# Kernel tuning notes

Measured on AMD Instinct MI355X. Metric: run time of the kernel, lower is better.

## Reference

```python
import jax, jax.numpy as jnp
import numpy as np

LAMB = 0.1
SIZE_AVERAGE = True


def setup_inputs() -> dict:
    key = jax.random.key(0)
    k1, k2 = jax.random.split(key)
    N, D = 8192, 4096
    inp = jax.random.normal(k1, (N, D), dtype=jnp.float32)
    target = jax.random.normal(k2, (N, D), dtype=jnp.float32)
    return {"input": inp, "target": target}


def _drae_loss(inp, target, lamb=LAMB, size_average=SIZE_AVERAGE):
    # Per-sample squared reconstruction error: Err[n] = sum_d (inp - target)^2
    err = (inp - target).reshape(inp.shape[0], -1)
    Err = jnp.sum(err * err, axis=1)                      # [N]
    N = Err.shape[0]
    sErr = jnp.sort(Err)                                  # ascending

    # Prefix sums replace the original O(N^2) Python scan.
    cs = jnp.cumsum(sErr)                                 # [N]
    cs2 = jnp.cumsum(sErr * sErr)                         # [N]
    total, total2 = cs[-1], cs2[-1]
    nf = jnp.asarray(N, sErr.dtype)
    allMean = total / nf
    Sb = total2 - nf * allMean * allMean                  # sum (e - allMean)^2

    # Candidate splits: inlier count k = 1..N-1 (loop index i = k-1).
    k = jnp.arange(1, N, dtype=sErr.dtype)                # [N-1]
    csk, cs2k = cs[:-1], cs2[:-1]
    Sw1 = cs2k - csk * csk / k                            # within-inlier scatter
    Sw2 = (total2 - cs2k) - (total - csk) ** 2 / (nf - k) # within-outlier scatter
    obj = (Sw1 + Sw2) / Sb                                # Fisher-style ratio

    i = jnp.argmin(obj)                                   # first min, like strict '<'
    optObj = obj[i]
    T = (i + 1).astype(sErr.dtype)                        # inlier count
    inlier_sum = cs[i]

    out = inlier_sum / T if size_average else inlier_sum
    return out + lamb * optObj


def reference(input, target):
    return _drae_loss(input, target)
```

## Files before the change

### kernel.cpp

```cpp
#include <hip/hip_runtime.h>

#define NROWS 8192
#define NCOLS 4096
#define LAMB  0.1

typedef unsigned int u32;
typedef unsigned long long u64;

__global__ __launch_bounds__(256) void rowerr_kernel(const float* __restrict__ inp,
                                                     const float* __restrict__ tgt,
                                                     float* __restrict__ err) {
    const int row = blockIdx.x;
    const float4* a = reinterpret_cast<const float4*>(inp + (size_t)row * NCOLS);
    const float4* b = reinterpret_cast<const float4*>(tgt + (size_t)row * NCOLS);
    const int t = threadIdx.x;

    float acc = 0.f;
#pragma unroll
    for (int c = 0; c < 4; ++c) {
        float4 va = a[t + c * 256];
        float4 vb = b[t + c * 256];
        float dx = va.x - vb.x;
        float dy = va.y - vb.y;
        float dz = va.z - vb.z;
        float dw = va.w - vb.w;
        acc += dx * dx + dy * dy + dz * dz + dw * dw;
    }

#pragma unroll
    for (int off = 32; off > 0; off >>= 1) acc += __shfl_down(acc, off, 64);

    __shared__ float ws[4];
    const int lane = t & 63, wv = t >> 6;
    if (lane == 0) ws[wv] = acc;
    __syncthreads();
    if (t == 0) err[row] = ws[0] + ws[1] + ws[2] + ws[3];
}

__device__ __forceinline__ double fastrcp(double x) {
    double r = (double)(1.0f / (float)x);
    r = r * (2.0 - x * r);
    r = r * (2.0 - x * r);
    return r;
}

__global__ __launch_bounds__(1024) void drae_kernel(const float* __restrict__ err,
                                                    float* __restrict__ out) {
    const int N = NROWS;
    __shared__ u32 bufA[NROWS];
    __shared__ u32 bufB[NROWS];
    __shared__ u32 hist[16 * 256];
    __shared__ u32 dtot[256], dbase[256];
    __shared__ u32 saux[4];
    __shared__ double auxX[16], auxT2[16], redH[16], redCs[16];
    __shared__ int    redIdx[16];

    const int tid  = threadIdx.x;
    const int lane = tid & 63, wv = tid >> 6;
    const u64 ltmask = (1ull << lane) - 1ull;

#pragma unroll
    for (int k = 0; k < 8; ++k) {
        const int i = tid + k * 1024;
        bufA[i] = __float_as_uint(err[i]);
    }

    u32* src = bufA;
    u32* dst = bufB;

    for (int pass = 0; pass < 4; ++pass) {
        const int shift = pass * 8;

        __syncthreads();
#pragma unroll
        for (int k = 0; k < 4; ++k) hist[tid + k * 1024] = 0;
        __syncthreads();

        u32 key[8], rnk[8];
#pragma unroll
        for (int r = 0; r < 8; ++r) key[r] = src[wv * 512 + r * 64 + lane];

#pragma unroll
        for (int r = 0; r < 8; ++r) {
            const u32 d = (key[r] >> shift) & 255u;
            u64 match = ~0ull;
#pragma unroll
            for (int b = 0; b < 8; ++b) {
                const u64 bb = __ballot((d >> b) & 1u);
                match &= ((d >> b) & 1u) ? bb : ~bb;
            }
            const int within = __popcll(match & ltmask);
            const int leader = __builtin_ctzll(match);
            const u32 base = hist[wv * 256 + d];
            rnk[r] = base + (u32)within;
            if (lane == leader) hist[wv * 256 + d] = base + (u32)__popcll(match);
        }
        __syncthreads();

        if (tid < 256) {
            u32 s = 0;
#pragma unroll
            for (int w = 0; w < 16; ++w) {
                const u32 t = hist[w * 256 + tid];
                hist[w * 256 + tid] = s;
                s += t;
            }
            dtot[tid] = s;
        }
        __syncthreads();

        u32 val = 0, incl = 0;
        if (tid < 256) {
            val  = dtot[tid];
            incl = val;
#pragma unroll
            for (int off = 1; off < 64; off <<= 1) {
                const u32 t = __shfl_up(incl, off, 64);
                if (lane >= off) incl += t;
            }
            if (lane == 63) saux[wv] = incl;
        }
        __syncthreads();
        if (tid < 256) {
            u32 add = 0;
#pragma unroll
            for (int w = 0; w < 4; ++w) if (w < wv) add += saux[w];
            dbase[tid] = incl - val + add;
        }
        __syncthreads();

#pragma unroll
        for (int r = 0; r < 8; ++r) {
            const u32 d = (key[r] >> shift) & 255u;
            dst[dbase[d] + hist[wv * 256 + d] + rnk[r]] = key[r];
        }

        u32* tmp = src; src = dst; dst = tmp;
    }
    __syncthreads();

    float v[8];
#pragma unroll
    for (int r = 0; r < 8; ++r) v[r] = __uint_as_float(src[(tid << 3) + r]);

    double sx = 0.0, sx2 = 0.0;
#pragma unroll
    for (int r = 0; r < 8; ++r) {
        sx  += (double)v[r];
        sx2 += (double)v[r] * (double)v[r];
    }

    double ix = sx;
#pragma unroll
    for (int off = 1; off < 64; off <<= 1) {
        double t1 = __shfl_up(ix, off, 64);
        if (lane >= off) ix += t1;
    }
    double t2 = sx2;
#pragma unroll
    for (int off = 32; off > 0; off >>= 1) t2 += __shfl_xor(t2, off, 64);

    if (lane == 63) auxX[wv]  = ix;
    if (lane == 0)  auxT2[wv] = t2;
    __syncthreads();

    double wOff1 = 0.0, total1 = 0.0, total2 = 0.0;
#pragma unroll
    for (int w = 0; w < 16; ++w) {
        const double a1 = auxX[w];
        if (w < wv) wOff1 += a1;
        total1 += a1;
        total2 += auxT2[w];
    }
    const double exc1 = wOff1 + (ix - sx);
    const double nf = (double)N;

    double run1 = exc1;
    double bestH = -1e300, bestCs = 0.0;
    int bestIdx = N;
#pragma unroll
    for (int r = 0; r < 8; ++r) {
        const int idx = (tid << 3) + r;
        run1 += (double)v[r];
        if (idx < N - 1) {
            const double kf  = (double)(idx + 1);
            const double rem = total1 - run1;
            const double h   = run1 * run1 * fastrcp(kf) +
                               rem  * rem  * fastrcp(nf - kf);
            if (h > bestH) { bestH = h; bestIdx = idx; bestCs = run1; }
        }
    }

#pragma unroll
    for (int off = 32; off > 0; off >>= 1) {
        const double oH   = __shfl_down(bestH, off, 64);
        const int    oIdx = __shfl_down(bestIdx, off, 64);
        const double oCs  = __shfl_down(bestCs, off, 64);
        if (oH > bestH || (oH == bestH && oIdx < bestIdx)) {
            bestH = oH; bestIdx = oIdx; bestCs = oCs;
        }
    }
    if (lane == 0) { redH[wv] = bestH; redIdx[wv] = bestIdx; redCs[wv] = bestCs; }
    __syncthreads();

    if (tid == 0) {
        double bH = redH[0], bCs = redCs[0];
        int bIdx = redIdx[0];
        for (int w = 1; w < 16; ++w) {
            if (redH[w] > bH || (redH[w] == bH && redIdx[w] < bIdx)) {
                bH = redH[w]; bIdx = redIdx[w]; bCs = redCs[w];
            }
        }
        const double Sb     = total2 - total1 * total1 / nf;
        const double optObj = (total2 - bH) / Sb;
        const double T      = (double)(bIdx + 1);
        out[0] = (float)(bCs / T + LAMB * optObj);
    }
}

extern "C" void kernel_launch(void* const* d_in, const int* in_sizes, int n_in,
                              void* d_out, int out_size, void* d_ws, size_t ws_size,
                              hipStream_t stream) {
    const float* inp = (const float*)d_in[0];
    const float* tgt = (const float*)d_in[1];
    float* errbuf = (float*)d_ws;

    rowerr_kernel<<<NROWS, 256, 0, stream>>>(inp, tgt, errbuf);
    drae_kernel<<<1, 1024, 0, stream>>>(errbuf, (float*)d_out);
}
```

Baseline: 74.04 us.

## Replace 4-pass LSD radix sort with single-pass bucket sort plus in-bucket rank

Replaces the four-pass 8-bit LSD radix sort of per-row errors with one pass that finds the min/max bit pattern, histograms keys into 2048 buckets with shared atomics, scatters them, then ranks each key inside its bucket by counting smaller keys. This removes most of the barrier-heavy passes and ballot-based digit matching in the single-block sort kernel. The risk is that the in-bucket ranking costs quadratic time in bucket size when buckets are skewed. The sort is a small share of the total, since the row-reduction kernel reading 256 MB dominates.

```diff
diff --git a/kernel.cpp b/kernel.cpp
--- a/kernel.cpp
+++ b/kernel.cpp
@@ -3,6 +3,7 @@
 #define NROWS 8192
 #define NCOLS 4096
 #define LAMB  0.1
+#define NBUCK 2048
 
 typedef unsigned int u32;
 typedef unsigned long long u64;
@@ -47,101 +48,98 @@
 __global__ __launch_bounds__(1024) void drae_kernel(const float* __restrict__ err,
                                                     float* __restrict__ out) {
     const int N = NROWS;
-    __shared__ u32 bufA[NROWS];
+    __shared__ u32 bufS[NROWS];
     __shared__ u32 bufB[NROWS];
-    __shared__ u32 hist[16 * 256];
-    __shared__ u32 dtot[256], dbase[256];
-    __shared__ u32 saux[4];
+    __shared__ u32 hist[NBUCK];
+    __shared__ u32 base2[NBUCK];
+    __shared__ u32 cnt2[NBUCK];
+    __shared__ u32 sMin[16], sMax[16], saux[16];
     __shared__ double auxX[16], auxT2[16], redH[16], redCs[16];
     __shared__ int    redIdx[16];
 
     const int tid  = threadIdx.x;
     const int lane = tid & 63, wv = tid >> 6;
-    const u64 ltmask = (1ull << lane) - 1ull;
-
-#pragma unroll
-    for (int k = 0; k < 8; ++k) {
-        const int i = tid + k * 1024;
-        bufA[i] = __float_as_uint(err[i]);
-    }
-
-    u32* src = bufA;
-    u32* dst = bufB;
-
-    for (int pass = 0; pass < 4; ++pass) {
-        const int shift = pass * 8;
-
-        __syncthreads();
-#pragma unroll
-        for (int k = 0; k < 4; ++k) hist[tid + k * 1024] = 0;
-        __syncthreads();
-
-        u32 key[8], rnk[8];
-#pragma unroll
-        for (int r = 0; r < 8; ++r) key[r] = src[wv * 512 + r * 64 + lane];
-
-#pragma unroll
-        for (int r = 0; r < 8; ++r) {
-            const u32 d = (key[r] >> shift) & 255u;
-            u64 match = ~0ull;
-#pragma unroll
-            for (int b = 0; b < 8; ++b) {
-                const u64 bb = __ballot((d >> b) & 1u);
-                match &= ((d >> b) & 1u) ? bb : ~bb;
-            }
-            const int within = __popcll(match & ltmask);
-            const int leader = __builtin_ctzll(match);
-            const u32 base = hist[wv * 256 + d];
-            rnk[r] = base + (u32)within;
-            if (lane == leader) hist[wv * 256 + d] = base + (u32)__popcll(match);
-        }
-        __syncthreads();
-
-        if (tid < 256) {
-            u32 s = 0;
-#pragma unroll
-            for (int w = 0; w < 16; ++w) {
-                const u32 t = hist[w * 256 + tid];
-                hist[w * 256 + tid] = s;
-                s += t;
-            }
-            dtot[tid] = s;
-        }
-        __syncthreads();
-
-        u32 val = 0, incl = 0;
-        if (tid < 256) {
-            val  = dtot[tid];
-            incl = val;
-#pragma unroll
-            for (int off = 1; off < 64; off <<= 1) {
-                const u32 t = __shfl_up(incl, off, 64);
-                if (lane >= off) incl += t;
-            }
-            if (lane == 63) saux[wv] = incl;
-        }
-        __syncthreads();
-        if (tid < 256) {
-            u32 add = 0;
-#pragma unroll
-            for (int w = 0; w < 4; ++w) if (w < wv) add += saux[w];
-            dbase[tid] = incl - val + add;
-        }
-        __syncthreads();
-
-#pragma unroll
-        for (int r = 0; r < 8; ++r) {
-            const u32 d = (key[r] >> shift) & 255u;
-            dst[dbase[d] + hist[wv * 256 + d] + rnk[r]] = key[r];
-        }
-
-        u32* tmp = src; src = dst; dst = tmp;
+
+    u32 bits[8];
+    u32 mn = 0xFFFFFFFFu, mx = 0u;
+#pragma unroll
+    for (int k = 0; k < 8; ++k) {
+        bits[k] = __float_as_uint(err[tid + k * 1024]);
+        mn = min(mn, bits[k]);
+        mx = max(mx, bits[k]);
+    }
+#pragma unroll
+    for (int off = 32; off > 0; off >>= 1) {
+        mn = min(mn, (u32)__shfl_xor((int)mn, off, 64));
+        mx = max(mx, (u32)__shfl_xor((int)mx, off, 64));
+    }
+    if (lane == 0) { sMin[wv] = mn; sMax[wv] = mx; }
+
+    hist[tid] = 0;
+    hist[tid + 1024] = 0;
+    __syncthreads();
+
+    u32 minb = sMin[0], maxb = sMax[0];
+#pragma unroll
+    for (int w = 1; w < 16; ++w) { minb = min(minb, sMin[w]); maxb = max(maxb, sMax[w]); }
+    const u32 range = maxb - minb;
+    const int nbits = 32 - __clz(range | 1u);
+    const int shift = (nbits > 11) ? (nbits - 11) : 0;
+
+    u32 bk[8];
+#pragma unroll
+    for (int k = 0; k < 8; ++k) {
+        bits[k] -= minb;
+        bk[k] = bits[k] >> shift;
+        atomicAdd(&hist[bk[k]], 1u);
+    }
+    __syncthreads();
+
+    const u32 c0 = hist[2 * tid], c1 = hist[2 * tid + 1];
+    const u32 tsum = c0 + c1;
+    u32 incl = tsum;
+#pragma unroll
+    for (int off = 1; off < 64; off <<= 1) {
+        const u32 t = __shfl_up(incl, off, 64);
+        if (lane >= off) incl += t;
+    }
+    if (lane == 63) saux[wv] = incl;
+    __syncthreads();
+    u32 add = 0;
+#pragma unroll
+    for (int w = 0; w < 16; ++w) if (w < wv) add += saux[w];
+    const u32 excl = add + incl - tsum;
+    base2[2 * tid] = excl;           base2[2 * tid + 1] = excl + c0;
+    cnt2[2 * tid]  = c0;             cnt2[2 * tid + 1]  = c1;
+    hist[2 * tid]  = excl;           hist[2 * tid + 1]  = excl + c0;
+    __syncthreads();
+
+    u32 myq[8];
+#pragma unroll
+    for (int k = 0; k < 8; ++k) {
+        const u32 p = atomicAdd(&hist[bk[k]], 1u);
+        myq[k] = p - base2[bk[k]];
+        bufB[p] = bits[k];
+    }
+    __syncthreads();
+
+#pragma unroll
+    for (int k = 0; k < 8; ++k) {
+        const u32 s = base2[bk[k]];
+        const u32 c = cnt2[bk[k]];
+        const u32 ki = bits[k];
+        u32 r = 0;
+        for (u32 q = 0; q < c; ++q) {
+            const u32 v = bufB[s + q];
+            r += (v < ki || (v == ki && q < myq[k])) ? 1u : 0u;
+        }
+        bufS[s + r] = ki;
     }
     __syncthreads();
 
     float v[8];
 #pragma unroll
-    for (int r = 0; r < 8; ++r) v[r] = __uint_as_float(src[(tid << 3) + r]);
+    for (int r = 0; r < 8; ++r) v[r] = __uint_as_float(bufS[(tid << 3) + r] + minb);
 
     double sx = 0.0, sx2 = 0.0;
 #pragma unroll
```

After: 67.06 us. -9.4%, faster.
